# Performance work log

Measured on AMD Instinct MI355X. Metric: run time of the kernel, lower is better.

Reference implementation:

```python
import jax, jax.numpy as jnp
import numpy as np

L = 10  # lattice_size


def _wilson_plaquette_loop(field, x):
    # Faithful translation of compute_wilson_loop: product of exp(plaquette) over 6 (mu,nu) pairs.
    coords = x[0, :4].astype(jnp.int32) % L
    loop = jnp.ones((1,), dtype=field.dtype)
    for mu in range(4):
        for nu in range(mu + 1, 4):
            pos = coords
            link1 = field[pos[0], pos[1], pos[2], mu]
            pos = pos.at[mu].set((pos[mu] + 1) % L)
            link2 = field[pos[0], pos[1], pos[2], nu]
            pos = pos.at[nu].set((pos[nu] + 1) % L)
            link3 = -field[pos[0], pos[1], pos[2], mu]
            pos = pos.at[mu].add(-1)  # original has no mod here
            link4 = -field[coords[0], coords[1], coords[2], nu]
            loop = loop * jnp.exp(link1 + link2 + link3 - (-link4) + 0.0 if False else link1 + link2 + link3 + link4)
    return loop


def setup_inputs() -> dict:
    key = jax.random.key(0)
    ks = jax.random.split(key, 20)
    s = 0.02  # scale weights to keep activations numerically sane
    d = jnp.float32
    return {
        'x': jax.random.normal(ks[0], (16384, 4), d),
        'field': jax.random.normal(ks[1], (L, L, L, 4), d),
        'fw1': jax.random.normal(ks[2], (4, 2048), d) * s,
        'fb1': jax.random.normal(ks[3], (2048,), d) * s,
        'fw2': jax.random.normal(ks[4], (2048, 4096), d) * s,
        'fb2': jax.random.normal(ks[5], (4096,), d) * s,
        'ww1': jax.random.normal(ks[6], (4096, 2048), d) * s,
        'wb1': jax.random.normal(ks[7], (2048,), d) * s,
        'ww2': jax.random.normal(ks[8], (2048, 1024), d) * s,
        'wb2': jax.random.normal(ks[9], (1024,), d) * s,
        'ww3': jax.random.normal(ks[10], (1024, 1), d) * s,
        'wb3': jax.random.normal(ks[11], (1,), d) * s,
        'tw1': jax.random.normal(ks[12], (4096, 2048), d) * s,
        'tb1': jax.random.normal(ks[13], (2048,), d) * s,
        'tw2': jax.random.normal(ks[14], (2048, 1), d) * s,
        'tb2': jax.random.normal(ks[15], (1,), d) * s,
    }


def reference(x, field, fw1, fb1, fw2, fb2, ww1, wb1, ww2, wb2, ww3, wb3, tw1, tb1, tw2, tb2):
    x4 = x[:, :4]
    h = jnp.maximum(x4 @ fw1 + fb1, 0.0)
    field_output = h @ fw2 + fb2                       # [B, dim]
    plaq = _wilson_plaquette_loop(field, x4)           # [1] (computed in torch forward, not returned)
    w = jnp.maximum(field_output @ ww1 + wb1, 0.0)
    w = jnp.maximum(w @ ww2 + wb2, 0.0)
    wilson_output = w @ ww3 + wb3                      # [B, 1]
    t = jnp.maximum(field_output @ tw1 + tb1, 0.0)
    topology_output = t @ tw2 + tb2                    # [B, 1]
    return field_output, wilson_output, topology_output, plaq
```

## Files before the change

kernel.cpp:

```cpp
#include <hip/hip_runtime.h>

#define L 10

using bf16x8 = __attribute__((ext_vector_type(8))) __bf16;
using u16x8  = __attribute__((ext_vector_type(8))) unsigned short;
using f32x4  = __attribute__((ext_vector_type(4))) float;

__device__ __forceinline__ unsigned short f2bf(float f) {
  unsigned int u = __float_as_uint(f);
  u += 0x7FFFu + ((u >> 16) & 1u);
  return (unsigned short)(u >> 16);
}
__device__ __forceinline__ float bf2f(unsigned short h) {
  return __uint_as_float(((unsigned int)h) << 16);
}

__global__ void plaq_kernel(const float* __restrict__ x,
                            const float* __restrict__ field,
                            float* __restrict__ out) {
  if (threadIdx.x != 0 || blockIdx.x != 0) return;
  int c[4];
#pragma unroll
  for (int i = 0; i < 4; ++i) {
    int v = (int)x[i];
    v %= L; if (v < 0) v += L;
    c[i] = v;
  }
  float S = 0.f;
  for (int mu = 0; mu < 4; ++mu)
    for (int nu = mu + 1; nu < 4; ++nu) {
      int p[4] = {c[0], c[1], c[2], c[3]};
      float l1 = field[((p[0]*L + p[1])*L + p[2])*4 + mu];
      p[mu] = (p[mu] + 1) % L;
      float l2 = field[((p[0]*L + p[1])*L + p[2])*4 + nu];
      p[nu] = (p[nu] + 1) % L;
      float l3 = field[((p[0]*L + p[1])*L + p[2])*4 + mu];
      float l4 = field[((c[0]*L + c[1])*L + c[2])*4 + nu];
      S += l1 + l2 - l3 - l4;
    }
  out[0] = expf(S);
}

__global__ void fc1_kernel(const float* __restrict__ x,
                           const float* __restrict__ fw1,
                           const float* __restrict__ fb1,
                           unsigned short* __restrict__ h) {
  const int N = 2048;
  int idx = blockIdx.x * blockDim.x + threadIdx.x;
  int m  = idx >> 8;
  int n0 = (idx & 255) * 8;
  float4 xv = *(const float4*)(x + (size_t)m * 4);
  unsigned short o[8];
#pragma unroll
  for (int j = 0; j < 8; ++j) {
    int n = n0 + j;
    float s = fb1[n] + xv.x * fw1[n] + xv.y * fw1[N + n]
                     + xv.z * fw1[2*N + n] + xv.w * fw1[3*N + n];
    o[j] = f2bf(fmaxf(s, 0.f));
  }
  *(u16x8*)(h + (size_t)m * N + n0) = *(const u16x8*)o;
}

__global__ void transpose_bf16_kernel(const float* __restrict__ W,
                                      unsigned short* __restrict__ WT,
                                      int K, int N) {
  __shared__ float tile[32][33];
  int n0 = blockIdx.x * 32, k0 = blockIdx.y * 32;
  int tx = threadIdx.x, ty = threadIdx.y;
#pragma unroll
  for (int i = 0; i < 32; i += 8)
    tile[ty + i][tx] = W[(size_t)(k0 + ty + i) * N + n0 + tx];
  __syncthreads();
#pragma unroll
  for (int i = 0; i < 32; i += 8)
    WT[(size_t)(n0 + ty + i) * K + k0 + tx] = f2bf(tile[tx][ty + i]);
}

__global__ void cast_bf16_kernel(const float* __restrict__ in,
                                 unsigned short* __restrict__ out) {
  size_t i = ((size_t)blockIdx.x * blockDim.x + threadIdx.x) * 8;
  unsigned short o[8];
#pragma unroll
  for (int j = 0; j < 8; ++j) o[j] = f2bf(in[i + j]);
  *(u16x8*)(out + i) = *(const u16x8*)o;
}

__global__ void biascat_kernel(const unsigned short* __restrict__ catT,
                               const float* __restrict__ fb2,
                               const float* __restrict__ wb1,
                               const float* __restrict__ tb1,
                               float* __restrict__ out) {
  int w    = blockIdx.x * 4 + (threadIdx.x >> 6);
  int lane = threadIdx.x & 63;
  if (w < 4096) { if (lane == 0) out[w] = fb2[w]; return; }
  int m = w - 4096;
  const unsigned short* row = catT + (size_t)m * 4096;
  float s = 0.f;
  for (int k = lane * 8; k < 4096; k += 512) {
    u16x8 v = *(const u16x8*)(row + k);
#pragma unroll
    for (int j = 0; j < 8; ++j) s += bf2f(v[j]) * fb2[k + j];
  }
#pragma unroll
  for (int off = 32; off; off >>= 1) s += __shfl_down(s, off);
  if (lane == 0) out[w] = s + (m < 2048 ? wb1[m] : tb1[m - 2048]);
}

__global__ __launch_bounds__(256, 2)
void gemm128_kernel(const unsigned short* __restrict__ A,
                    const unsigned short* __restrict__ BT,
                    unsigned short* __restrict__ outB,
                    int N, int K) {
  constexpr int BK = 64;
  __shared__ unsigned short As[128 * BK];
  __shared__ unsigned short Bs[128 * BK];

  const int bm = blockIdx.x, bn = blockIdx.y;
  const int tid = threadIdx.x;
  const int wid = tid >> 6, lane = tid & 63;
  const int wr = wid >> 1, wc = wid & 1;
  const int lr = lane & 15, lg = lane >> 4;

  f32x4 acc[4][4];
#pragma unroll
  for (int m = 0; m < 4; ++m)
#pragma unroll
    for (int n = 0; n < 4; ++n) acc[m][n] = (f32x4)0.f;

  const int srow = wid * 32 + (lane >> 3);
  const int scol = (lane & 7) * 8;
  const unsigned short* Ag = A  + (size_t)(bm * 128 + srow) * K + scol;
  const unsigned short* Bg = BT + (size_t)(bn * 128 + srow) * K + scol;

  for (int kt = 0; kt < K; kt += BK) {
#pragma unroll
    for (int i = 0; i < 4; ++i) {
      __builtin_amdgcn_global_load_lds(
          (const __attribute__((address_space(1))) unsigned int*)(Ag + (size_t)i * 8 * K + kt),
          (__attribute__((address_space(3))) unsigned int*)&As[wid * 2048 + i * 512],
          16, 0, 0);
      __builtin_amdgcn_global_load_lds(
          (const __attribute__((address_space(1))) unsigned int*)(Bg + (size_t)i * 8 * K + kt),
          (__attribute__((address_space(3))) unsigned int*)&Bs[wid * 2048 + i * 512],
          16, 0, 0);
    }
    __syncthreads();
#pragma unroll
    for (int kk = 0; kk < 2; ++kk) {
      u16x8 af[4], bf[4];
#pragma unroll
      for (int m = 0; m < 4; ++m)
        af[m] = *(const u16x8*)&As[(wr * 64 + m * 16 + lr) * BK + kk * 32 + lg * 8];
#pragma unroll
      for (int n = 0; n < 4; ++n)
        bf[n] = *(const u16x8*)&Bs[(wc * 64 + n * 16 + lr) * BK + kk * 32 + lg * 8];
#pragma unroll
      for (int m = 0; m < 4; ++m)
#pragma unroll
        for (int n = 0; n < 4; ++n)
          acc[m][n] = __builtin_amdgcn_mfma_f32_16x16x32_bf16(
              __builtin_bit_cast(bf16x8, af[m]),
              __builtin_bit_cast(bf16x8, bf[n]),
              acc[m][n], 0, 0, 0);
    }
    __syncthreads();
  }

  const int rowBase = bm * 128 + wr * 64 + lg * 4;
  const int colBase = bn * 128 + wc * 64 + lr;
#pragma unroll
  for (int n = 0; n < 4; ++n) {
    int col = colBase + n * 16;
#pragma unroll
    for (int m = 0; m < 4; ++m) {
      int row = rowBase + m * 16;
#pragma unroll
      for (int j = 0; j < 4; ++j)
        outB[(size_t)(row + j) * N + col] = f2bf(acc[m][n][j]);
    }
  }
}

#define GLL(gp, lp)                                                            \
  __builtin_amdgcn_global_load_lds(                                            \
      (const __attribute__((address_space(1))) unsigned int*)(gp),             \
      (__attribute__((address_space(3))) unsigned int*)(lp), 16, 0, 0)

#define DSREAD(dst, addr)                                                      \
  asm volatile("ds_read_b128 %0, %1" : "=v"(dst) : "v"(addr))

#define LGKM(n)                                                                \
  do { asm volatile("s_waitcnt lgkmcnt(" #n ")" ::: "memory");                 \
       __builtin_amdgcn_sched_barrier(0); } while (0)

#define FENCE() asm volatile("" ::: "memory")

extern __shared__ char lds_raw[];

__global__ __launch_bounds__(512)
void gemm256_kernel(const unsigned short* __restrict__ A,
                    const unsigned short* __restrict__ BT,
                    const float* __restrict__ bias,
                    float* __restrict__ outF,
                    unsigned short* __restrict__ outB,
                    int lda, int K, int NF, int NB, int nFtiles, int gmx) {
  const int NT = K >> 5;

  const int nwg = gridDim.x;
  const int q = nwg >> 3, r = nwg & 7;
  const int xcd = blockIdx.x & 7, lid = blockIdx.x >> 3;
  const int wg2 = (xcd < r ? xcd * (q + 1) : r * (q + 1) + (xcd - r) * q) + lid;
  const int bm = wg2 % gmx, bn = wg2 / gmx;

  const int tid  = threadIdx.x;
  const int wid  = tid >> 6, lane = tid & 63;
  const int wr   = wid >> 2, wc = wid & 3;
  const int lr   = lane & 15, lg = lane >> 4;

  const int srow = tid >> 2;
  const int scol = ((tid & 3) ^ ((tid >> 3) & 3)) * 8;
  const unsigned short* agp0 = A  + (size_t)(bm * 256 + srow) * lda + scol;
  const unsigned short* agp1 = agp0 + (size_t)128 * lda;
  const unsigned short* bgp0 = BT + (size_t)(bn * 256 + srow) * K + scol;
  const unsigned short* bgp1 = bgp0 + (size_t)128 * K;

  const int chunk = lg ^ ((lr >> 1) & 3);
  const unsigned ldsbase = (unsigned)(uintptr_t)&lds_raw[0];
  const unsigned aoff = (unsigned)((wr * 128 + lr) * 64 + chunk * 16);
  const unsigned boff = (unsigned)(16384 + (wc * 64 + lr) * 64 + chunk * 16);

  f32x4 acc[8][4];
#pragma unroll
  for (int m = 0; m < 8; ++m)
#pragma unroll
    for (int n = 0; n < 4; ++n) acc[m][n] = (f32x4)0.f;

#define STAGE_A(tt) do { unsigned so = (unsigned)(((tt) & 3) << 15);           \
    GLL(agp0 + (size_t)(tt) * 32, lds_raw + so + tid * 16);                    \
    GLL(agp1 + (size_t)(tt) * 32, lds_raw + so + 8192 + tid * 16); } while (0)
#define STAGE_B(tt) do { unsigned so = (unsigned)(((tt) & 3) << 15);           \
    GLL(bgp0 + (size_t)(tt) * 32, lds_raw + so + 16384 + tid * 16);            \
    GLL(bgp1 + (size_t)(tt) * 32, lds_raw + so + 24576 + tid * 16); } while (0)

  STAGE_A(0); STAGE_B(0); STAGE_A(1); STAGE_B(1); STAGE_A(2); STAGE_B(2);

  for (int t = 0; t < NT; ++t) {
    const int rem = NT - 1 - t;
    if (rem >= 2)      asm volatile("s_waitcnt vmcnt(8)" ::: "memory");
    else if (rem == 1) asm volatile("s_waitcnt vmcnt(4)" ::: "memory");
    else               asm volatile("s_waitcnt vmcnt(0)" ::: "memory");
    FENCE(); __builtin_amdgcn_s_barrier(); FENCE();
    __builtin_amdgcn_sched_barrier(0);

    const unsigned sbase = ldsbase + (unsigned)((t & 3) << 15);

    u16x8 b[4], a[8];
    DSREAD(b[0], sbase + boff);
    DSREAD(b[1], sbase + boff + 1024);
    DSREAD(b[2], sbase + boff + 2048);
    DSREAD(b[3], sbase + boff + 3072);
    DSREAD(a[0], sbase + aoff);
    DSREAD(a[1], sbase + aoff + 1024);
    DSREAD(a[2], sbase + aoff + 2048);
    DSREAD(a[3], sbase + aoff + 3072);
    DSREAD(a[4], sbase + aoff + 4096);
    DSREAD(a[5], sbase + aoff + 5120);
    DSREAD(a[6], sbase + aoff + 6144);
    DSREAD(a[7], sbase + aoff + 7168);
    if (t + 3 < NT) { STAGE_A(t + 3); STAGE_B(t + 3); }

    __builtin_amdgcn_s_setprio(1);
#define CLUSTER(m, g)                                                          \
    LGKM(g);                                                                   \
    acc[m][0] = __builtin_amdgcn_mfma_f32_16x16x32_bf16(                       \
        __builtin_bit_cast(bf16x8, a[m]), __builtin_bit_cast(bf16x8, b[0]),    \
        acc[m][0], 0, 0, 0);                                                   \
    acc[m][1] = __builtin_amdgcn_mfma_f32_16x16x32_bf16(                       \
        __builtin_bit_cast(bf16x8, a[m]), __builtin_bit_cast(bf16x8, b[1]),    \
        acc[m][1], 0, 0, 0);                                                   \
    acc[m][2] = __builtin_amdgcn_mfma_f32_16x16x32_bf16(                       \
        __builtin_bit_cast(bf16x8, a[m]), __builtin_bit_cast(bf16x8, b[2]),    \
        acc[m][2], 0, 0, 0);                                                   \
    acc[m][3] = __builtin_amdgcn_mfma_f32_16x16x32_bf16(                       \
        __builtin_bit_cast(bf16x8, a[m]), __builtin_bit_cast(bf16x8, b[3]),    \
        acc[m][3], 0, 0, 0)

    CLUSTER(0, 7);
    CLUSTER(1, 6);
    CLUSTER(2, 5);
    CLUSTER(3, 4);
    CLUSTER(4, 3);
    CLUSTER(5, 2);
    CLUSTER(6, 1);
    CLUSTER(7, 0);
#undef CLUSTER
    __builtin_amdgcn_s_setprio(0);
    __builtin_amdgcn_sched_barrier(0);
  }
#undef STAGE_A
#undef STAGE_B

  const int rowBase = bm * 256 + wr * 128 + lg * 4;
  const int colBase = bn * 256 + wc * 64 + lr;
  if (bn < nFtiles) {
#pragma unroll
    for (int n = 0; n < 4; ++n) {
      int col = colBase + n * 16;
      float bv = bias[col];
#pragma unroll
      for (int m = 0; m < 8; ++m) {
        int row = rowBase + m * 16;
#pragma unroll
        for (int j = 0; j < 4; ++j)
          outF[(size_t)(row + j) * NF + col] = acc[m][n][j] + bv;
      }
    }
  } else {
    const int colB = colBase - nFtiles * 256;
#pragma unroll
    for (int n = 0; n < 4; ++n) {
      int col = colB + n * 16;
      float bv = bias[colBase + n * 16];
#pragma unroll
      for (int m = 0; m < 8; ++m) {
        int row = rowBase + m * 16;
#pragma unroll
        for (int j = 0; j < 4; ++j)
          outB[(size_t)(row + j) * NB + col] = f2bf(fmaxf(acc[m][n][j] + bv, 0.f));
      }
    }
  }
}

__global__ void gemv_kernel(const unsigned short* __restrict__ Abf,
                            const float* __restrict__ wvec,
                            const float* __restrict__ bias,
                            float* __restrict__ out, int K, int lda) {
  int row  = blockIdx.x * 4 + (threadIdx.x >> 6);
  int lane = threadIdx.x & 63;
  const unsigned short* ap = Abf + (size_t)row * lda;
  float s = 0.f;
  for (int k = lane * 8; k < K; k += 512) {
    u16x8 v = *(const u16x8*)(ap + k);
#pragma unroll
    for (int j = 0; j < 8; ++j) s += bf2f(v[j]) * wvec[k + j];
  }
#pragma unroll
  for (int off = 32; off; off >>= 1) s += __shfl_down(s, off);
  if (lane == 0) out[row] = s + bias[0];
}

extern "C" void kernel_launch(void* const* d_in, const int* in_sizes, int n_in,
                              void* d_out, int out_size, void* d_ws, size_t ws_size,
                              hipStream_t stream) {
  const float* x     = (const float*)d_in[0];
  const float* field = (const float*)d_in[1];
  const float* fw1   = (const float*)d_in[2];
  const float* fb1   = (const float*)d_in[3];
  const float* fw2   = (const float*)d_in[4];
  const float* fb2   = (const float*)d_in[5];
  const float* ww1   = (const float*)d_in[6];
  const float* wb1   = (const float*)d_in[7];
  const float* ww2   = (const float*)d_in[8];
  const float* wb2   = (const float*)d_in[9];
  const float* ww3   = (const float*)d_in[10];
  const float* wb3   = (const float*)d_in[11];
  const float* tw1   = (const float*)d_in[12];
  const float* tb1   = (const float*)d_in[13];
  const float* tw2   = (const float*)d_in[14];
  const float* tb2   = (const float*)d_in[15];

  const int M = 16384;
  float* outF    = (float*)d_out;
  float* outWil  = outF + (size_t)M * 4096;
  float* outTop  = outWil + M;
  float* outPlaq = outTop + M;

  char* ws = (char*)d_ws;
  const size_t MB = 1048576;
  unsigned short* hbuf    = (unsigned short*)(ws);
  unsigned short* catbuf  = (unsigned short*)(ws + 64  * MB);
  unsigned short* catT    = (unsigned short*)(ws + 192 * MB);
  unsigned short* w2buf   = (unsigned short*)(ws + 192 * MB);
  unsigned short* fw2T    = (unsigned short*)(ws + 224 * MB);
  unsigned short* W2catT  = (unsigned short*)(ws + 240 * MB);
  unsigned short* BTcat   = fw2T;
  unsigned short* fw2bf   = (unsigned short*)(ws + 256 * MB);
  unsigned short* ww2T    = (unsigned short*)(ws + 272 * MB);
  float*          biascat = (float*)(ws + 276 * MB);

  const int SMEM = 131072;
  (void)hipFuncSetAttribute((const void*)gemm256_kernel,
                            hipFuncAttributeMaxDynamicSharedMemorySize, SMEM);

  hipLaunchKernelGGL(plaq_kernel, dim3(1), dim3(64), 0, stream, x, field, outPlaq);
  hipLaunchKernelGGL(fc1_kernel, dim3(16384), dim3(256), 0, stream, x, fw1, fb1, hbuf);
  hipLaunchKernelGGL(transpose_bf16_kernel, dim3(128, 64), dim3(32, 8), 0, stream,
                     fw2, fw2T, 2048, 4096);
  hipLaunchKernelGGL(cast_bf16_kernel, dim3(4096), dim3(256), 0, stream, fw2, fw2bf);
  hipLaunchKernelGGL(transpose_bf16_kernel, dim3(64, 128), dim3(32, 8), 0, stream,
                     ww1, catT, 4096, 2048);
  hipLaunchKernelGGL(transpose_bf16_kernel, dim3(64, 128), dim3(32, 8), 0, stream,
                     tw1, catT + (size_t)2048 * 4096, 4096, 2048);
  hipLaunchKernelGGL(transpose_bf16_kernel, dim3(32, 64), dim3(32, 8), 0, stream,
                     ww2, ww2T, 2048, 1024);
  hipLaunchKernelGGL(biascat_kernel, dim3(2048), dim3(256), 0, stream,
                     catT, fb2, wb1, tb1, biascat);

  hipLaunchKernelGGL(gemm128_kernel, dim3(32, 16), dim3(256), 0, stream,
                     catT, fw2bf, W2catT, 2048, 4096);

  hipLaunchKernelGGL(gemm256_kernel, dim3(64 * 32), dim3(512), SMEM, stream,
                     hbuf, BTcat, biascat, outF, catbuf,
                     2048, 2048, 4096, 4096, 16, 64);

  hipLaunchKernelGGL(gemm256_kernel, dim3(64 * 4), dim3(512), SMEM, stream,
                     catbuf, ww2T, wb2, (float*)nullptr, w2buf,
                     4096, 2048, 0, 1024, 0, 64);

  hipLaunchKernelGGL(gemv_kernel, dim3(4096), dim3(256), 0, stream,
                     w2buf, ww3, wb3, outWil, 1024, 1024);
  hipLaunchKernelGGL(gemv_kernel, dim3(4096), dim3(256), 0, stream,
                     catbuf + 2048, tw2, tb2, outTop, 2048, 4096);

  (void)in_sizes; (void)n_in; (void)out_size; (void)ws_size;
}
```

Before: 898.5 us.

## Restructure GEMM main loop into half-tile staged double-buffered K=64 pipeline

Replaces the 4-stage K=32 ring buffer with two K=64 LDS buffers. Each buffer is loaded in half-tile pieces interleaved with 16-MFMA quads and barriers, in a ping-pong schedule with an 8-wide XOR swizzle. The aim is to hide global-to-LDS loads and LDS reads behind MFMA work while issuing fewer, larger loads per iteration. It adds many more barriers per iteration and assumes K is a multiple of 128, and the hand-tuned waitcnt counts must match the loads exactly.

Result: slower. 3.044 ms (+238.8%).

```diff
diff --git a/kernel.cpp b/kernel.cpp
--- a/kernel.cpp
+++ b/kernel.cpp
@@ -193,7 +193,9 @@
   do { asm volatile("s_waitcnt lgkmcnt(" #n ")" ::: "memory");                 \
        __builtin_amdgcn_sched_barrier(0); } while (0)
 
+#define VMC(n)  asm volatile("s_waitcnt vmcnt(" #n ")" ::: "memory")
 #define FENCE() asm volatile("" ::: "memory")
+#define BAR()   do { FENCE(); __builtin_amdgcn_s_barrier(); FENCE(); } while (0)
 
 extern __shared__ char lds_raw[];
 
@@ -204,7 +206,7 @@
                     float* __restrict__ outF,
                     unsigned short* __restrict__ outB,
                     int lda, int K, int NF, int NB, int nFtiles, int gmx) {
-  const int NT = K >> 5;
+  const int NI = K >> 7;
 
   const int nwg = gridDim.x;
   const int q = nwg >> 3, r = nwg & 7;
@@ -217,17 +219,36 @@
   const int wr   = wid >> 2, wc = wid & 3;
   const int lr   = lane & 15, lg = lane >> 4;
 
-  const int srow = tid >> 2;
-  const int scol = ((tid & 3) ^ ((tid >> 3) & 3)) * 8;
-  const unsigned short* agp0 = A  + (size_t)(bm * 256 + srow) * lda + scol;
-  const unsigned short* agp1 = agp0 + (size_t)128 * lda;
-  const unsigned short* bgp0 = BT + (size_t)(bn * 256 + srow) * K + scol;
-  const unsigned short* bgp1 = bgp0 + (size_t)128 * K;
-
-  const int chunk = lg ^ ((lr >> 1) & 3);
-  const unsigned ldsbase = (unsigned)(uintptr_t)&lds_raw[0];
-  const unsigned aoff = (unsigned)((wr * 128 + lr) * 64 + chunk * 16);
-  const unsigned boff = (unsigned)(16384 + (wc * 64 + lr) * 64 + chunk * 16);
+  const int scol = ((tid & 7) ^ ((tid >> 3) & 7)) * 8;
+  const unsigned short* aS = A  + (size_t)(bm * 256 + (tid >> 3)) * lda + scol;
+  const unsigned short* bS = BT + (size_t)(bn * 256 + (tid >> 3)) * K  + scol;
+  const size_t sA64 = (size_t)64 * lda, sB64 = (size_t)64 * K;
+
+#define STG_A(tile, half, g)                                                   \
+  GLL(aS + (size_t)((half)*2 + (g)) * sA64 + (size_t)(tile) * 64,              \
+      lds_raw + (((tile)&1) << 16) + (half)*16384 + (g)*8192 + tid*16)
+#define STG_B(tile, half, g)                                                   \
+  GLL(bS + (size_t)((half)*2 + (g)) * sB64 + (size_t)(tile) * 64,              \
+      lds_raw + (((tile)&1) << 16) + 32768 + (half)*16384 + (g)*8192 + tid*16)
+#define SHA(tile, half) do { STG_A(tile, half, 0); STG_A(tile, half, 1); } while (0)
+#define SHB(tile, half) do { STG_B(tile, half, 0); STG_B(tile, half, 1); } while (0)
+
+  const unsigned ldsb = (unsigned)(uintptr_t)&lds_raw[0];
+  const unsigned ck0  = (unsigned)(((lg)     ^ (lr & 7)) * 16);
+  const unsigned ck1  = (unsigned)(((4 + lg) ^ (lr & 7)) * 16);
+  const unsigned aB0  = ldsb + (unsigned)(wr * 16384 + lr * 128);
+  const unsigned bB0  = ldsb + (unsigned)(32768 + (wc >> 1) * 16384 +
+                                          (wc & 1) * 8192 + lr * 128);
+#define RD_A(dst, buf, m, ck) DSREAD(dst, aB0 + ((buf) << 16) + (m)*2048 + (ck))
+#define RD_B(dst, buf, n, ck) DSREAD(dst, bB0 + ((buf) << 16) + (n)*2048 + (ck))
+#define R8(BS, AS, buf, ck) do {                                               \
+    RD_B(BS[0], buf, 0, ck); RD_B(BS[1], buf, 1, ck);                          \
+    RD_B(BS[2], buf, 2, ck); RD_B(BS[3], buf, 3, ck);                          \
+    RD_A(AS[0], buf, 0, ck); RD_A(AS[1], buf, 1, ck);                          \
+    RD_A(AS[2], buf, 2, ck); RD_A(AS[3], buf, 3, ck); } while (0)
+#define R4(AS, buf, ck) do {                                                   \
+    RD_A(AS[0], buf, 4, ck); RD_A(AS[1], buf, 5, ck);                          \
+    RD_A(AS[2], buf, 6, ck); RD_A(AS[3], buf, 7, ck); } while (0)
 
   f32x4 acc[8][4];
 #pragma unroll
@@ -235,70 +256,67 @@
 #pragma unroll
     for (int n = 0; n < 4; ++n) acc[m][n] = (f32x4)0.f;
 
-#define STAGE_A(tt) do { unsigned so = (unsigned)(((tt) & 3) << 15);           \
-    GLL(agp0 + (size_t)(tt) * 32, lds_raw + so + tid * 16);                    \
-    GLL(agp1 + (size_t)(tt) * 32, lds_raw + so + 8192 + tid * 16); } while (0)
-#define STAGE_B(tt) do { unsigned so = (unsigned)(((tt) & 3) << 15);           \
-    GLL(bgp0 + (size_t)(tt) * 32, lds_raw + so + 16384 + tid * 16);            \
-    GLL(bgp1 + (size_t)(tt) * 32, lds_raw + so + 24576 + tid * 16); } while (0)
-
-  STAGE_A(0); STAGE_B(0); STAGE_A(1); STAGE_B(1); STAGE_A(2); STAGE_B(2);
-
-  for (int t = 0; t < NT; ++t) {
-    const int rem = NT - 1 - t;
-    if (rem >= 2)      asm volatile("s_waitcnt vmcnt(8)" ::: "memory");
-    else if (rem == 1) asm volatile("s_waitcnt vmcnt(4)" ::: "memory");
-    else               asm volatile("s_waitcnt vmcnt(0)" ::: "memory");
-    FENCE(); __builtin_amdgcn_s_barrier(); FENCE();
-    __builtin_amdgcn_sched_barrier(0);
-
-    const unsigned sbase = ldsbase + (unsigned)((t & 3) << 15);
-
-    u16x8 b[4], a[8];
-    DSREAD(b[0], sbase + boff);
-    DSREAD(b[1], sbase + boff + 1024);
-    DSREAD(b[2], sbase + boff + 2048);
-    DSREAD(b[3], sbase + boff + 3072);
-    DSREAD(a[0], sbase + aoff);
-    DSREAD(a[1], sbase + aoff + 1024);
-    DSREAD(a[2], sbase + aoff + 2048);
-    DSREAD(a[3], sbase + aoff + 3072);
-    DSREAD(a[4], sbase + aoff + 4096);
-    DSREAD(a[5], sbase + aoff + 5120);
-    DSREAD(a[6], sbase + aoff + 6144);
-    DSREAD(a[7], sbase + aoff + 7168);
-    if (t + 3 < NT) { STAGE_A(t + 3); STAGE_B(t + 3); }
-
-    __builtin_amdgcn_s_setprio(1);
-#define CLUSTER(m, g)                                                          \
-    LGKM(g);                                                                   \
-    acc[m][0] = __builtin_amdgcn_mfma_f32_16x16x32_bf16(                       \
-        __builtin_bit_cast(bf16x8, a[m]), __builtin_bit_cast(bf16x8, b[0]),    \
-        acc[m][0], 0, 0, 0);                                                   \
-    acc[m][1] = __builtin_amdgcn_mfma_f32_16x16x32_bf16(                       \
-        __builtin_bit_cast(bf16x8, a[m]), __builtin_bit_cast(bf16x8, b[1]),    \
-        acc[m][1], 0, 0, 0);                                                   \
-    acc[m][2] = __builtin_amdgcn_mfma_f32_16x16x32_bf16(                       \
-        __builtin_bit_cast(bf16x8, a[m]), __builtin_bit_cast(bf16x8, b[2]),    \
-        acc[m][2], 0, 0, 0);                                                   \
-    acc[m][3] = __builtin_amdgcn_mfma_f32_16x16x32_bf16(                       \
-        __builtin_bit_cast(bf16x8, a[m]), __builtin_bit_cast(bf16x8, b[3]),    \
-        acc[m][3], 0, 0, 0)
-
-    CLUSTER(0, 7);
-    CLUSTER(1, 6);
-    CLUSTER(2, 5);
-    CLUSTER(3, 4);
-    CLUSTER(4, 3);
-    CLUSTER(5, 2);
-    CLUSTER(6, 1);
-    CLUSTER(7, 0);
-#undef CLUSTER
-    __builtin_amdgcn_s_setprio(0);
-    __builtin_amdgcn_sched_barrier(0);
-  }
-#undef STAGE_A
-#undef STAGE_B
+#define QUAD(mb, AS, BS) do {                                                  \
+    __builtin_amdgcn_s_setprio(1);                                             \
+    _Pragma("unroll")                                                          \
+    for (int _m = 0; _m < 4; ++_m)                                             \
+      _Pragma("unroll")                                                        \
+      for (int _n = 0; _n < 4; ++_n)                                           \
+        acc[(mb) + _m][_n] = __builtin_amdgcn_mfma_f32_16x16x32_bf16(          \
+            __builtin_bit_cast(bf16x8, AS[_m]),                                \
+            __builtin_bit_cast(bf16x8, BS[_n]), acc[(mb) + _m][_n], 0, 0, 0);  \
+    __builtin_amdgcn_s_setprio(0);                                             \
+  } while (0)
+
+  u16x8 bA[4], bX[4], aA[4], aX[4];
+
+  SHB(0, 0); SHB(0, 1); SHA(0, 0); SHA(0, 1);
+  SHB(1, 0);
+  VMC(2); BAR();
+  R8(bA, aA, 0, ck0);
+
+  for (int i = 0; i < NI; ++i) {
+    const int t1 = 2 * i + 1;
+    const bool nx = (i + 1 < NI);
+    SHB(t1, 1); SHA(t1, 0); SHA(t1, 1);
+    R4(aX, 0, ck0);
+    LGKM(4); QUAD(0, aA, bA); BAR();
+    R8(bX, aA, 0, ck1);
+    LGKM(8); QUAD(4, aX, bA); BAR();
+    R4(aX, 0, ck1);
+    LGKM(4); QUAD(0, aA, bX); BAR();
+    if (nx) { SHB(2 * i + 2, 0); SHB(2 * i + 2, 1); VMC(4); }
+    else VMC(0);
+    BAR();
+    R8(bA, aA, 1, ck0);
+    LGKM(8); QUAD(4, aX, bX); BAR();
+    if (nx) { SHA(2 * i + 2, 0); SHA(2 * i + 2, 1); }
+    R4(aX, 1, ck0);
+    LGKM(4); QUAD(0, aA, bA); BAR();
+    R8(bX, aA, 1, ck1);
+    LGKM(8); QUAD(4, aX, bA); BAR();
+    R4(aX, 1, ck1);
+    LGKM(4); QUAD(0, aA, bX); BAR();
+    if (nx) {
+      SHB(2 * i + 3, 0);
+      VMC(2); BAR();
+      R8(bA, aA, 0, ck0);
+      LGKM(8);
+    } else {
+      VMC(0); BAR();
+      LGKM(0);
+    }
+    QUAD(4, aX, bX); BAR();
+  }
+#undef STG_A
+#undef STG_B
+#undef SHA
+#undef SHB
+#undef RD_A
+#undef RD_B
+#undef R8
+#undef R4
+#undef QUAD
 
   const int rowBase = bm * 256 + wr * 128 + lg * 4;
   const int colBase = bn * 256 + wc * 64 + lr;
```

## Fuse final GEMV heads into GEMM epilogues via shuffle reduction and atomics

Applied to the files above, without the earlier changes.

Removes the two standalone GEMV kernels for the wilson and topology heads. Their dot products against ww3 and tw2 are now computed in the gemm256 epilogue: each tile applies bias and ReLU, reduces across lanes with shuffles, and atomically adds a partial sum per row into outputs pre-initialised with the bias. This avoids writing and re-reading the bf16 intermediate activations (the topology half of catbuf and the ww2 output). The cost is atomic contention on 16384 rows and a reduction order that is no longer deterministic.

New measurement: 874.0 us. -2.7%, faster.

```diff
diff --git a/kernel.cpp b/kernel.cpp
--- a/kernel.cpp
+++ b/kernel.cpp
@@ -39,6 +39,14 @@
       S += l1 + l2 - l3 - l4;
     }
   out[0] = expf(S);
+}
+
+__global__ void init_heads_kernel(float* __restrict__ outWil,
+                                  float* __restrict__ outTop,
+                                  const float* __restrict__ wb3,
+                                  const float* __restrict__ tb2) {
+  int i = blockIdx.x * blockDim.x + threadIdx.x;
+  if (i < 16384) { outWil[i] = wb3[0]; outTop[i] = tb2[0]; }
 }
 
 __global__ void fc1_kernel(const float* __restrict__ x,
@@ -203,7 +211,10 @@
                     const float* __restrict__ bias,
                     float* __restrict__ outF,
                     unsigned short* __restrict__ outB,
-                    int lda, int K, int NF, int NB, int nFtiles, int gmx) {
+                    const float* __restrict__ hvec,
+                    float* __restrict__ hout,
+                    int lda, int K, int NF, int NB,
+                    int nFtiles, int nHtiles, int gmx) {
   const int NT = K >> 5;
 
   const int nwg = gridDim.x;
@@ -315,7 +326,7 @@
           outF[(size_t)(row + j) * NF + col] = acc[m][n][j] + bv;
       }
     }
-  } else {
+  } else if (bn < nHtiles) {
     const int colB = colBase - nFtiles * 256;
 #pragma unroll
     for (int n = 0; n < 4; ++n) {
@@ -329,25 +340,31 @@
           outB[(size_t)(row + j) * NB + col] = f2bf(fmaxf(acc[m][n][j] + bv, 0.f));
       }
     }
-  }
-}
-
-__global__ void gemv_kernel(const unsigned short* __restrict__ Abf,
-                            const float* __restrict__ wvec,
-                            const float* __restrict__ bias,
-                            float* __restrict__ out, int K, int lda) {
-  int row  = blockIdx.x * 4 + (threadIdx.x >> 6);
-  int lane = threadIdx.x & 63;
-  const unsigned short* ap = Abf + (size_t)row * lda;
-  float s = 0.f;
-  for (int k = lane * 8; k < K; k += 512) {
-    u16x8 v = *(const u16x8*)(ap + k);
-#pragma unroll
-    for (int j = 0; j < 8; ++j) s += bf2f(v[j]) * wvec[k + j];
-  }
-#pragma unroll
-  for (int off = 32; off; off >>= 1) s += __shfl_down(s, off);
-  if (lane == 0) out[row] = s + bias[0];
+  } else {
+    const int hcol0 = colBase - nHtiles * 256;
+    float bv[4], hv[4];
+#pragma unroll
+    for (int n = 0; n < 4; ++n) {
+      bv[n] = bias[colBase + n * 16];
+      hv[n] = hvec[hcol0 + n * 16];
+    }
+#pragma unroll
+    for (int m = 0; m < 8; ++m) {
+#pragma unroll
+      for (int j = 0; j < 4; ++j) {
+        float s = 0.f;
+#pragma unroll
+        for (int n = 0; n < 4; ++n)
+          s += fmaxf(acc[m][n][j] + bv[n], 0.f) * hv[n];
+        s += __shfl_xor(s, 1);
+        s += __shfl_xor(s, 2);
+        s += __shfl_xor(s, 4);
+        s += __shfl_xor(s, 8);
+        if (lr == 0)
+          atomicAdd(&hout[rowBase + m * 16 + j], s);
+      }
+    }
+  }
 }
 
 extern "C" void kernel_launch(void* const* d_in, const int* in_sizes, int n_in,
@@ -381,7 +398,6 @@
   unsigned short* hbuf    = (unsigned short*)(ws);
   unsigned short* catbuf  = (unsigned short*)(ws + 64  * MB);
   unsigned short* catT    = (unsigned short*)(ws + 192 * MB);
-  unsigned short* w2buf   = (unsigned short*)(ws + 192 * MB);
   unsigned short* fw2T    = (unsigned short*)(ws + 224 * MB);
   unsigned short* W2catT  = (unsigned short*)(ws + 240 * MB);
   unsigned short* BTcat   = fw2T;
@@ -394,6 +410,8 @@
                             hipFuncAttributeMaxDynamicSharedMemorySize, SMEM);
 
   hipLaunchKernelGGL(plaq_kernel, dim3(1), dim3(64), 0, stream, x, field, outPlaq);
+  hipLaunchKernelGGL(init_heads_kernel, dim3(64), dim3(256), 0, stream,
+                     outWil, outTop, wb3, tb2);
   hipLaunchKernelGGL(fc1_kernel, dim3(16384), dim3(256), 0, stream, x, fw1, fb1, hbuf);
   hipLaunchKernelGGL(transpose_bf16_kernel, dim3(128, 64), dim3(32, 8), 0, stream,
                      fw2, fw2T, 2048, 4096);
@@ -411,17 +429,13 @@
                      catT, fw2bf, W2catT, 2048, 4096);
 
   hipLaunchKernelGGL(gemm256_kernel, dim3(64 * 32), dim3(512), SMEM, stream,
-                     hbuf, BTcat, biascat, outF, catbuf,
-                     2048, 2048, 4096, 4096, 16, 64);
+                     hbuf, BTcat, biascat, outF, catbuf, tw2, outTop,
+                     2048, 2048, 4096, 2048, 16, 24, 64);
 
   hipLaunchKernelGGL(gemm256_kernel, dim3(64 * 4), dim3(512), SMEM, stream,
-                     catbuf, ww2T, wb2, (float*)nullptr, w2buf,
-                     4096, 2048, 0, 1024, 0, 64);
-
-  hipLaunchKernelGGL(gemv_kernel, dim3(4096), dim3(256), 0, stream,
-                     w2buf, ww3, wb3, outWil, 1024, 1024);
-  hipLaunchKernelGGL(gemv_kernel, dim3(4096), dim3(256), 0, stream,
-                     catbuf + 2048, tw2, tb2, outTop, 2048, 4096);
+                     catbuf, ww2T, wb2, (float*)nullptr, (unsigned short*)nullptr,
+                     ww3, outWil,
+                     2048, 2048, 0, 0, 0, 0, 64);
 
   (void)in_sizes; (void)n_in; (void)out_size; (void)ws_size;
 }
```
